# Kernel tuning notes

Hardware: AMD Instinct MI355X
Metric: run time of the kernel (lower is better)

## Reference

```python
import jax, jax.numpy as jnp
import numpy as np

K = 7  # kernel_size from init


def setup_inputs() -> dict:
    key = jax.random.key(0)
    ks = jax.random.split(key, 4)
    B, C, H, W = 8, 64, 384, 384
    x = jax.random.normal(ks[0], (B, C, H, W), dtype=jnp.float32)
    w1 = jax.random.normal(ks[1], (16, C), dtype=jnp.float32) * (1.0 / np.sqrt(C))
    b1 = jnp.zeros((16,), dtype=jnp.float32)
    w2 = jax.random.normal(ks[2], (3, 16), dtype=jnp.float32) * 0.25
    b2 = jnp.zeros((3,), dtype=jnp.float32)
    return {"x": x, "w1": w1, "b1": b1, "w2": w2, "b2": b2}


def reference(x, w1, b1, w2, b2):
    B, C, H, W = x.shape
    # param predictor: global avg pool -> 1x1 conv (dense) -> SiLU -> 1x1 conv (dense)
    pooled = x.mean(axis=(2, 3))                       # [B, C]
    h = jax.nn.silu(pooled @ w1.T + b1)                # [B, 16]
    p = h @ w2.T + b2                                  # [B, 3]
    sigma = jax.nn.softplus(p[:, 0])                   # [B]
    dx = jnp.tanh(p[:, 1]) * 2.0
    dy = jnp.tanh(p[:, 2]) * 2.0
    # per-sample Gaussian kernels, vectorized over batch
    coords = jnp.arange(K, dtype=x.dtype)
    gy, gx = jnp.meshgrid(coords, coords, indexing="ij")  # [K, K]
    cx = (K - 1) / 2.0 + dx                            # [B]
    cy = (K - 1) / 2.0 + dy
    g = jnp.exp(-((gx[None] - cx[:, None, None]) ** 2 + (gy[None] - cy[:, None, None]) ** 2)
                / (2.0 * sigma[:, None, None] ** 2))   # [B, K, K]
    g = g / g.sum(axis=(1, 2), keepdims=True)
    # depthwise conv with per-sample kernel via groups = B*C
    kernels = jnp.broadcast_to(g[:, None], (B, C, K, K)).reshape(B * C, 1, K, K)
    out = jax.lax.conv_general_dilated(
        x.reshape(1, B * C, H, W), kernels,
        window_strides=(1, 1), padding=[(K // 2, K // 2)] * 2,
        feature_group_count=B * C,
        dimension_numbers=("NCHW", "OIHW", "NCHW"))
    return out.reshape(B, C, H, W)
```

## Files before the change

kernel.cpp:

```cpp
#include <hip/hip_runtime.h>
#include <math.h>

#define IMG_W 384
#define IMG_H 384
#define IMG_HW (IMG_W * IMG_H)
#define N_IMG 512
#define N_CH 64
#define N_B 8
#define POOL_PARTS 4

__global__ __launch_bounds__(256) void pool_kernel(const float* __restrict__ x,
                                                   float* __restrict__ partial) {
    const int blk = blockIdx.x;
    const int bc = blk >> 2;
    const int part = blk & 3;
    const float4* xp = (const float4*)(x + (size_t)bc * IMG_HW + part * (IMG_HW / POOL_PARTS));
    const int t = threadIdx.x;
    float s0 = 0.f, s1 = 0.f;
    #pragma unroll
    for (int k = 0; k < 36; k += 2) {
        float4 a = xp[t + k * 256];
        float4 b = xp[t + (k + 1) * 256];
        s0 += (a.x + a.y) + (a.z + a.w);
        s1 += (b.x + b.y) + (b.z + b.w);
    }
    float s = s0 + s1;
    #pragma unroll
    for (int off = 32; off > 0; off >>= 1) s += __shfl_down(s, off, 64);
    __shared__ float red[4];
    if ((t & 63) == 0) red[t >> 6] = s;
    __syncthreads();
    if (t == 0) partial[blk] = (red[0] + red[1]) + (red[2] + red[3]);
}

__global__ __launch_bounds__(512) void params_kernel(const float* __restrict__ partial,
                              const float* __restrict__ w1, const float* __restrict__ b1,
                              const float* __restrict__ w2, const float* __restrict__ b2,
                              float* __restrict__ guv) {
    __shared__ float pooled[N_IMG];
    const int t = threadIdx.x;
    {
        float4 pp = *(const float4*)(partial + t * 4);
        pooled[t] = (pp.x + pp.y + pp.z + pp.w) * (1.0f / (float)IMG_HW);
    }
    __syncthreads();
    const int b = t;
    if (b >= N_B) return;
    const float* P = &pooled[b * N_CH];
    float h[16];
    #pragma unroll
    for (int j = 0; j < 16; ++j) {
        float acc = b1[j];
        for (int c = 0; c < N_CH; ++c) acc += P[c] * w1[j * N_CH + c];
        h[j] = acc / (1.f + expf(-acc));
    }
    float p[3];
    #pragma unroll
    for (int k = 0; k < 3; ++k) {
        float acc = b2[k];
        #pragma unroll
        for (int j = 0; j < 16; ++j) acc += h[j] * w2[k * 16 + j];
        p[k] = acc;
    }
    float sigma = (p[0] > 20.f) ? p[0] : log1pf(expf(p[0]));
    float dx = tanhf(p[1]) * 2.f;
    float dy = tanhf(p[2]) * 2.f;
    float cx = 3.f + dx, cy = 3.f + dy;
    float inv2s2 = 1.f / (2.f * sigma * sigma);
    float u[7], v[7], su = 0.f, sv = 0.f;
    #pragma unroll
    for (int i = 0; i < 7; ++i) { float d = (float)i - cx; u[i] = expf(-d * d * inv2s2); su += u[i]; }
    #pragma unroll
    for (int j = 0; j < 7; ++j) { float d = (float)j - cy; v[j] = expf(-d * d * inv2s2); sv += v[j]; }
    float rsu = 1.f / su, rsv = 1.f / sv;
    #pragma unroll
    for (int i = 0; i < 7; ++i) guv[b * 14 + i] = u[i] * rsu;
    #pragma unroll
    for (int j = 0; j < 7; ++j) guv[b * 14 + 7 + j] = v[j] * rsv;
}

#define BANDS 2
#define BAND_ROWS 192
#define GROUP_ROWS 48
#define NITER 27
#define LROW 392

__global__ __launch_bounds__(384) void conv_kernel(const float* __restrict__ x,
                                                   const float* __restrict__ guv,
                                                   float* __restrict__ out) {
    __shared__ float buf[2][8][LROW];
    const int tid = threadIdx.x;
    const int tx = tid % 96;
    const int ty = tid / 96;
    const int blk = blockIdx.x;
    const int bc = blk >> 1;
    const int band = blk & 1;
    const int b = bc >> 6;
    const float* img = x + (size_t)bc * IMG_HW;
    float* oimg = out + (size_t)bc * IMG_HW;
    const int base4 = 4 * tx;
    const int gbase = band * BAND_ROWS + ty * GROUP_ROWS;

    float u[7], v[7];
    #pragma unroll
    for (int i = 0; i < 7; ++i) { u[i] = guv[b * 14 + i]; v[i] = guv[b * 14 + 7 + i]; }

    if (tid < 128) {
        int r = tid >> 3;
        int p = tid & 7;
        int col = (p < 4) ? p : (384 + p);
        buf[r >> 3][r & 7][col] = 0.f;
    }

    #pragma unroll
    for (int k = 0; k < 2; ++k) {
        int s = ty + 4 * k;
        int g = s >> 1, sub = s & 1;
        int row = band * BAND_ROWS + g * GROUP_ROWS - 3 + sub;
        float4 val = make_float4(0.f, 0.f, 0.f, 0.f);
        if (row >= 0 && row < IMG_H) val = *(const float4*)(img + row * IMG_W + base4);
        *(float4*)&buf[0][s][4 + base4] = val;
    }
    __syncthreads();

    float4 h[6];
    #pragma unroll
    for (int k = 0; k < 6; ++k) h[k] = make_float4(0.f, 0.f, 0.f, 0.f);

    for (int it = 0; it < NITER; ++it) {
        float4 nv[2];
        const bool have_next = (it + 1 < NITER);
        if (have_next) {
            #pragma unroll
            for (int k = 0; k < 2; ++k) {
                int s = ty + 4 * k;
                int g = s >> 1, sub = s & 1;
                int row = band * BAND_ROWS + g * GROUP_ROWS + 2 * (it + 1) - 3 + sub;
                nv[k] = make_float4(0.f, 0.f, 0.f, 0.f);
                if (row >= 0 && row < IMG_H) nv[k] = *(const float4*)(img + row * IMG_W + base4);
            }
        }
        const float (*cb)[LROW] = buf[it & 1];
        #pragma unroll
        for (int r = 0; r < 2; ++r) {
            const float* rp = &cb[ty * 2 + r][base4];
            float4 a  = *(const float4*)(rp);
            float4 bq = *(const float4*)(rp + 4);
            float4 cq = *(const float4*)(rp + 8);
            float wv[12] = {a.x, a.y, a.z, a.w, bq.x, bq.y, bq.z, bq.w,
                            cq.x, cq.y, cq.z, cq.w};
            float4 hn;
            hn.x = u[0]*wv[1] + u[1]*wv[2] + u[2]*wv[3] + u[3]*wv[4] + u[4]*wv[5] + u[5]*wv[6] + u[6]*wv[7];
            hn.y = u[0]*wv[2] + u[1]*wv[3] + u[2]*wv[4] + u[3]*wv[5] + u[4]*wv[6] + u[5]*wv[7] + u[6]*wv[8];
            hn.z = u[0]*wv[3] + u[1]*wv[4] + u[2]*wv[5] + u[3]*wv[6] + u[4]*wv[7] + u[5]*wv[8] + u[6]*wv[9];
            hn.w = u[0]*wv[4] + u[1]*wv[5] + u[2]*wv[6] + u[3]*wv[7] + u[4]*wv[8] + u[5]*wv[9] + u[6]*wv[10];
            if (it >= 3) {
                const int y = gbase + 2 * (it - 3) + r;
                float4 o;
                o.x = v[0]*h[0].x + v[1]*h[1].x + v[2]*h[2].x + v[3]*h[3].x + v[4]*h[4].x + v[5]*h[5].x + v[6]*hn.x;
                o.y = v[0]*h[0].y + v[1]*h[1].y + v[2]*h[2].y + v[3]*h[3].y + v[4]*h[4].y + v[5]*h[5].y + v[6]*hn.y;
                o.z = v[0]*h[0].z + v[1]*h[1].z + v[2]*h[2].z + v[3]*h[3].z + v[4]*h[4].z + v[5]*h[5].z + v[6]*hn.z;
                o.w = v[0]*h[0].w + v[1]*h[1].w + v[2]*h[2].w + v[3]*h[3].w + v[4]*h[4].w + v[5]*h[5].w + v[6]*hn.w;
                *(float4*)(oimg + y * IMG_W + base4) = o;
            }
            #pragma unroll
            for (int k2 = 0; k2 < 5; ++k2) h[k2] = h[k2 + 1];
            h[5] = hn;
        }
        if (have_next) {
            float (*bn)[LROW] = buf[(it + 1) & 1];
            #pragma unroll
            for (int k = 0; k < 2; ++k) {
                int s = ty + 4 * k;
                *(float4*)&bn[s][4 + base4] = nv[k];
            }
        }
        __syncthreads();
    }
}

extern "C" void kernel_launch(void* const* d_in, const int* in_sizes, int n_in,
                              void* d_out, int out_size, void* d_ws, size_t ws_size,
                              hipStream_t stream) {
    const float* x  = (const float*)d_in[0];
    const float* w1 = (const float*)d_in[1];
    const float* b1 = (const float*)d_in[2];
    const float* w2 = (const float*)d_in[3];
    const float* b2 = (const float*)d_in[4];
    float* outp = (float*)d_out;

    float* partial = (float*)d_ws;
    float* guv     = partial + 2048;

    pool_kernel<<<N_IMG * POOL_PARTS, 256, 0, stream>>>(x, partial);
    params_kernel<<<1, 512, 0, stream>>>(partial, w1, b1, w2, b2, guv);
    conv_kernel<<<N_IMG * BANDS, 384, 0, stream>>>(x, guv, outp);
}
```

Baseline: 588.9 us.

## Fuse pooling and param kernels, reverse pool order, nontemporal conv stores

Merges the pool and params kernels into one launch: the last block to finish, detected with an atomic counter, computes the Gaussian parameters. Pool blocks now walk the images in reverse, so the images read last stay in cache and the conv kernel, which starts from the first image, can reuse them. The conv output uses nontemporal stores to avoid evicting input from cache, and the row loop is unrolled by 3. It adds a memset launch and atomic/fence overhead, and the reverse-order cache reuse depends on L2/MALL capacity.

```diff
diff --git a/kernel.cpp b/kernel.cpp
--- a/kernel.cpp
+++ b/kernel.cpp
@@ -8,11 +8,18 @@
 #define N_CH 64
 #define N_B 8
 #define POOL_PARTS 4
-
-__global__ __launch_bounds__(256) void pool_kernel(const float* __restrict__ x,
-                                                   float* __restrict__ partial) {
+#define POOL_BLOCKS (N_IMG * POOL_PARTS)
+
+typedef float f4v __attribute__((ext_vector_type(4)));
+
+__global__ __launch_bounds__(256) void pool_params_kernel(
+        const float* __restrict__ x,
+        const float* __restrict__ w1, const float* __restrict__ b1,
+        const float* __restrict__ w2, const float* __restrict__ b2,
+        float* __restrict__ partial, float* __restrict__ guv,
+        unsigned int* __restrict__ counter) {
     const int blk = blockIdx.x;
-    const int bc = blk >> 2;
+    const int bc = (N_IMG - 1) - (blk >> 2);
     const int part = blk & 3;
     const float4* xp = (const float4*)(x + (size_t)bc * IMG_HW + part * (IMG_HW / POOL_PARTS));
     const int t = threadIdx.x;
@@ -28,20 +35,25 @@
     #pragma unroll
     for (int off = 32; off > 0; off >>= 1) s += __shfl_down(s, off, 64);
     __shared__ float red[4];
+    __shared__ unsigned int lastflag;
     if ((t & 63) == 0) red[t >> 6] = s;
     __syncthreads();
-    if (t == 0) partial[blk] = (red[0] + red[1]) + (red[2] + red[3]);
-}
-
-__global__ __launch_bounds__(512) void params_kernel(const float* __restrict__ partial,
-                              const float* __restrict__ w1, const float* __restrict__ b1,
-                              const float* __restrict__ w2, const float* __restrict__ b2,
-                              float* __restrict__ guv) {
+    if (t == 0) {
+        partial[bc * 4 + part] = (red[0] + red[1]) + (red[2] + red[3]);
+        __threadfence();
+        unsigned int old = atomicAdd(counter, 1u);
+        lastflag = (old == POOL_BLOCKS - 1) ? 1u : 0u;
+    }
+    __syncthreads();
+    if (!lastflag) return;
+
+    __threadfence();
     __shared__ float pooled[N_IMG];
-    const int t = threadIdx.x;
-    {
-        float4 pp = *(const float4*)(partial + t * 4);
-        pooled[t] = (pp.x + pp.y + pp.z + pp.w) * (1.0f / (float)IMG_HW);
+    #pragma unroll
+    for (int i = 0; i < 2; ++i) {
+        int img = t + i * 256;
+        float4 pp = *(const float4*)(partial + img * 4);
+        pooled[img] = (pp.x + pp.y + pp.z + pp.w) * (1.0f / (float)IMG_HW);
     }
     __syncthreads();
     const int b = t;
@@ -127,6 +139,7 @@
     #pragma unroll
     for (int k = 0; k < 6; ++k) h[k] = make_float4(0.f, 0.f, 0.f, 0.f);
 
+    #pragma unroll 3
     for (int it = 0; it < NITER; ++it) {
         float4 nv[2];
         const bool have_next = (it + 1 < NITER);
@@ -156,12 +169,12 @@
             hn.w = u[0]*wv[4] + u[1]*wv[5] + u[2]*wv[6] + u[3]*wv[7] + u[4]*wv[8] + u[5]*wv[9] + u[6]*wv[10];
             if (it >= 3) {
                 const int y = gbase + 2 * (it - 3) + r;
-                float4 o;
+                f4v o;
                 o.x = v[0]*h[0].x + v[1]*h[1].x + v[2]*h[2].x + v[3]*h[3].x + v[4]*h[4].x + v[5]*h[5].x + v[6]*hn.x;
                 o.y = v[0]*h[0].y + v[1]*h[1].y + v[2]*h[2].y + v[3]*h[3].y + v[4]*h[4].y + v[5]*h[5].y + v[6]*hn.y;
                 o.z = v[0]*h[0].z + v[1]*h[1].z + v[2]*h[2].z + v[3]*h[3].z + v[4]*h[4].z + v[5]*h[5].z + v[6]*hn.z;
                 o.w = v[0]*h[0].w + v[1]*h[1].w + v[2]*h[2].w + v[3]*h[3].w + v[4]*h[4].w + v[5]*h[5].w + v[6]*hn.w;
-                *(float4*)(oimg + y * IMG_W + base4) = o;
+                __builtin_nontemporal_store(o, (f4v*)(oimg + y * IMG_W + base4));
             }
             #pragma unroll
             for (int k2 = 0; k2 < 5; ++k2) h[k2] = h[k2 + 1];
@@ -191,8 +204,10 @@
 
     float* partial = (float*)d_ws;
     float* guv     = partial + 2048;
-
-    pool_kernel<<<N_IMG * POOL_PARTS, 256, 0, stream>>>(x, partial);
-    params_kernel<<<1, 512, 0, stream>>>(partial, w1, b1, w2, b2, guv);
+    unsigned int* counter = (unsigned int*)(guv + 112);
+
+    hipMemsetAsync(counter, 0, sizeof(unsigned int), stream);
+    pool_params_kernel<<<POOL_BLOCKS, 256, 0, stream>>>(x, w1, b1, w2, b2,
+                                                        partial, guv, counter);
     conv_kernel<<<N_IMG * BANDS, 384, 0, stream>>>(x, guv, outp);
 }
```

Result: slower. 662.2 us (+12.4%).
